# Kernel optimization log

Measured on AMD Instinct MI355X. Metric: run time of the kernel, lower is better.

## Reference

```python
import jax, jax.numpy as jnp
import numpy as np

EPS = 1e-05  # config.norm_eps
C = 4        # len('qkvm')

def setup_inputs() -> dict:
    key = jax.random.key(0)
    k1, k2, k3 = jax.random.split(key, 3)
    B, T, D = 4, 4096, 4096
    L_TOT = 48  # (lidx+2)*C with lidx=10
    x = jax.random.normal(k1, (B, T, D), dtype=jnp.float32)
    # torch Linear weights are [out_features, in_features]
    W1 = jax.random.normal(k2, (L_TOT, D), dtype=jnp.float32) * (D ** -0.5)
    W2 = jax.random.normal(k3, (L_TOT, L_TOT), dtype=jnp.float32) * (L_TOT ** -0.5)
    return {"x": x, "W1": W1, "W2": W2}

def reference(x, W1, W2):
    # RMSNorm without scale
    var = jnp.mean(x * x, axis=-1, keepdims=True)
    xn = x * jax.lax.rsqrt(var + EPS)                      # [B, T, D]
    h = jnp.einsum('btd,ld->btl', xn, W1)                  # [B, T, l]
    dw = jnp.einsum('btk,lk->btl', jax.nn.gelu(h, approximate=False), W2)
    B, T, Ltot = dw.shape
    # rearrange 'B T (C L) -> C B T L'
    return jnp.transpose(dw.reshape(B, T, C, Ltot // C), (2, 0, 1, 3))
```

## Files before the change

kernel.cpp:

```cpp
#include <hip/hip_runtime.h>
#include <hip/hip_bf16.h>

#define DDIM 4096
#define LTOT 48

typedef __attribute__((ext_vector_type(4))) float f32x4;
typedef __attribute__((ext_vector_type(8))) short bf16x8;

__device__ __forceinline__ void gload_lds16(const void* g, void* l) {
    __builtin_amdgcn_global_load_lds(
        (const __attribute__((address_space(1))) void*)g,
        (__attribute__((address_space(3))) void*)l, 16, 0, 0);
}

__device__ __forceinline__ unsigned cvt_pk(float x, float y) {
    union { __hip_bfloat162 h; unsigned u; } c;
    c.h = __float22bfloat162_rn(make_float2(x, y));
    return c.u;
}

__global__ void w1cvt_kernel(const float* __restrict__ w1, ushort* __restrict__ w1b) {
    int i = blockIdx.x * 256 + threadIdx.x;
    union { float f; unsigned u; } v; v.f = w1[i];
    unsigned r = v.u + 0x7fffu + ((v.u >> 16) & 1u);
    w1b[i] = (ushort)(r >> 16);
}

__global__ __launch_bounds__(256, 2) void fused_kernel(
        const float* __restrict__ x,
        const ushort* __restrict__ w1b,
        const float* __restrict__ w2,
        float* __restrict__ out) {
    __shared__ __align__(1024) char smem[65536];
    __shared__ float ssw[4][32];
    __shared__ float scl[32];

    const int tid  = threadIdx.x;
    const int wave = tid >> 6;
    const int lane = tid & 63;
    const int rl   = lane & 15;
    const int kg   = lane >> 4;
    const int row0 = blockIdx.x * 32;
    const int kw   = wave * 1024;
    const int rot  = blockIdx.x & 15;

    char* wbase = smem + wave * 16384;

    int dso[2][2][2];
    #pragma unroll
    for (int T = 0; T < 2; ++T)
        #pragma unroll
        for (int h = 0; h < 2; ++h)
            #pragma unroll
            for (int p = 0; p < 2; ++p)
                dso[T][h][p] = (T * 16 + rl) * 256 + (((h * 8 + kg * 2 + p) ^ rl) << 4);

    auto stage = [&](int t) {
        const int kb = kw + ((t + rot) & 15) * 64;
        char* lb = wbase + (t & 1) * 8192;
        #pragma unroll
        for (int i = 0; i < 8; ++i) {
            int r    = i * 4 + kg;
            int blkg = rl ^ (r & 15);
            const float* src = x + (size_t)(row0 + r) * DDIM + kb + blkg * 4;
            gload_lds16(src, lb + i * 1024);
        }
    };

    auto loadB = [&](int s, bf16x8 (&bl)[6]) {
        const ushort* bp = w1b + (size_t)rl * DDIM + kw + ((s + rot) & 15) * 64 + kg * 8;
        #pragma unroll
        for (int n = 0; n < 3; ++n)
            #pragma unroll
            for (int h = 0; h < 2; ++h)
                bl[n * 2 + h] = *(const bf16x8*)(bp + n * 16 * DDIM + h * 32);
    };

    float ss0 = 0.f, ss1 = 0.f;
    f32x4 acc0[3] = {{0.f,0.f,0.f,0.f},{0.f,0.f,0.f,0.f},{0.f,0.f,0.f,0.f}};
    f32x4 acc1[3] = {{0.f,0.f,0.f,0.f},{0.f,0.f,0.f,0.f},{0.f,0.f,0.f,0.f}};
    bf16x8 bA[6], bB[6];

    stage(0); loadB(0, bA); stage(1);

    auto body = [&](int s, bf16x8 (&bu)[6], bf16x8 (&bl)[6]) {
        if (s == 0)       asm volatile("s_waitcnt vmcnt(14)" ::: "memory");
        else if (s == 15) asm volatile("s_waitcnt vmcnt(6)"  ::: "memory");
        else              asm volatile("s_waitcnt vmcnt(8)"  ::: "memory");
        char* lb = wbase + (s & 1) * 8192;
        f32x4 a[2][2][2];
        #pragma unroll
        for (int T = 0; T < 2; ++T)
            #pragma unroll
            for (int h = 0; h < 2; ++h)
                #pragma unroll
                for (int p = 0; p < 2; ++p)
                    a[T][h][p] = *(const f32x4*)(lb + dso[T][h][p]);
        if (s < 15) loadB(s + 1, bl);
        #pragma unroll
        for (int h = 0; h < 2; ++h) {
            f32x4 a0 = a[0][h][0], a1 = a[0][h][1];
            f32x4 c0 = a[1][h][0], c1 = a[1][h][1];
            ss0 = fmaf(a0.x, a0.x, ss0); ss0 = fmaf(a0.y, a0.y, ss0);
            ss0 = fmaf(a0.z, a0.z, ss0); ss0 = fmaf(a0.w, a0.w, ss0);
            ss0 = fmaf(a1.x, a1.x, ss0); ss0 = fmaf(a1.y, a1.y, ss0);
            ss0 = fmaf(a1.z, a1.z, ss0); ss0 = fmaf(a1.w, a1.w, ss0);
            ss1 = fmaf(c0.x, c0.x, ss1); ss1 = fmaf(c0.y, c0.y, ss1);
            ss1 = fmaf(c0.z, c0.z, ss1); ss1 = fmaf(c0.w, c0.w, ss1);
            ss1 = fmaf(c1.x, c1.x, ss1); ss1 = fmaf(c1.y, c1.y, ss1);
            ss1 = fmaf(c1.z, c1.z, ss1); ss1 = fmaf(c1.w, c1.w, ss1);
            union { bf16x8 v; unsigned u[4]; } af, ag;
            af.u[0] = cvt_pk(a0.x, a0.y); af.u[1] = cvt_pk(a0.z, a0.w);
            af.u[2] = cvt_pk(a1.x, a1.y); af.u[3] = cvt_pk(a1.z, a1.w);
            ag.u[0] = cvt_pk(c0.x, c0.y); ag.u[1] = cvt_pk(c0.z, c0.w);
            ag.u[2] = cvt_pk(c1.x, c1.y); ag.u[3] = cvt_pk(c1.z, c1.w);
            #pragma unroll
            for (int n = 0; n < 3; ++n) {
                acc0[n] = __builtin_amdgcn_mfma_f32_16x16x32_bf16(
                              af.v, bu[n * 2 + h], acc0[n], 0, 0, 0);
                acc1[n] = __builtin_amdgcn_mfma_f32_16x16x32_bf16(
                              ag.v, bu[n * 2 + h], acc1[n], 0, 0, 0);
            }
        }
        asm volatile("s_waitcnt lgkmcnt(0)" ::: "memory");
        if (s < 14) stage(s + 2);
    };

    for (int sp = 0; sp < 8; ++sp) {
        body(2 * sp,     bA, bB);
        body(2 * sp + 1, bB, bA);
    }

    ss0 += __shfl_xor(ss0, 16); ss0 += __shfl_xor(ss0, 32);
    ss1 += __shfl_xor(ss1, 16); ss1 += __shfl_xor(ss1, 32);
    if (lane < 16) { ssw[wave][lane] = ss0; ssw[wave][16 + lane] = ss1; }

    asm volatile("s_waitcnt vmcnt(0) lgkmcnt(0)" ::: "memory");
    __syncthreads();

    float* dots = (float*)smem;
    float* gbuf = (float*)(smem + 24576);
    float* w2s  = (float*)(smem + 30720);

    #pragma unroll
    for (int n = 0; n < 3; ++n)
        #pragma unroll
        for (int i = 0; i < 4; ++i) {
            dots[(wave * 32 + kg * 4 + i) * 48 + n * 16 + rl]      = acc0[n][i];
            dots[(wave * 32 + 16 + kg * 4 + i) * 48 + n * 16 + rl] = acc1[n][i];
        }
    for (int i = tid; i < LTOT * LTOT; i += 256) w2s[i] = w2[i];
    if (tid < 32) {
        float st = ssw[0][tid] + ssw[1][tid] + ssw[2][tid] + ssw[3][tid];
        scl[tid] = rsqrtf(st * (1.0f / (float)DDIM) + 1e-5f);
    }
    __syncthreads();

    #pragma unroll
    for (int i = 0; i < 6; ++i) {
        int v = tid + i * 256;
        int row = v / 48, col = v - row * 48;
        float d = dots[(0 * 32 + row) * 48 + col] + dots[(1 * 32 + row) * 48 + col]
                + dots[(2 * 32 + row) * 48 + col] + dots[(3 * 32 + row) * 48 + col];
        float h = d * scl[row];
        gbuf[row * 48 + col] = h * 0.5f * (1.0f + erff(h * 0.70710678118654752f));
    }
    __syncthreads();

    #pragma unroll
    for (int i = 0; i < 6; ++i) {
        int v = tid + i * 256;
        int row = v / 48, l = v - row * 48;
        float sacc = 0.f;
        #pragma unroll
        for (int k = 0; k < LTOT; ++k)
            sacc = fmaf(gbuf[row * 48 + k], w2s[l * LTOT + k], sacc);
        int rg = row0 + row;
        int b  = rg >> 12;
        int t  = rg & 4095;
        int c  = l / 12, j = l - c * 12;
        out[(((size_t)(c * 4 + b) * 4096 + t) * 12) + j] = sacc;
    }
}

extern "C" void kernel_launch(void* const* d_in, const int* in_sizes, int n_in,
                              void* d_out, int out_size, void* d_ws, size_t ws_size,
                              hipStream_t stream) {
    const float* x  = (const float*)d_in[0];
    const float* W1 = (const float*)d_in[1];
    const float* W2 = (const float*)d_in[2];
    float* out = (float*)d_out;
    ushort* w1b = (ushort*)d_ws;

    w1cvt_kernel<<<(LTOT * DDIM) / 256, 256, 0, stream>>>(W1, w1b);
    fused_kernel<<<16384 / 32, 256, 0, stream>>>(x, w1b, W2, out);
}
```

Before: 58.07 us.

## Stage x tiles through registers into a single-buffered LDS bridge

Replaces the direct global-to-LDS async loads and the double-buffered 64 KB LDS staging with register prefetch: two chunks of x are held in registers and written into a smaller per-wave LDS buffer after each compute step. W1 fragments are now loaded directly in each iteration instead of being prefetched one step ahead, and the hand-written waitcnt instructions are dropped in favour of compiler scheduling. The smaller LDS footprint is meant to allow more resident blocks per CU. The cost is more VGPR pressure from the register staging buffers, extra LDS write instructions, and W1 load latency that is no longer hidden by a prefetch.

```diff
diff --git a/kernel.cpp b/kernel.cpp
--- a/kernel.cpp
+++ b/kernel.cpp
@@ -6,12 +6,6 @@
 
 typedef __attribute__((ext_vector_type(4))) float f32x4;
 typedef __attribute__((ext_vector_type(8))) short bf16x8;
-
-__device__ __forceinline__ void gload_lds16(const void* g, void* l) {
-    __builtin_amdgcn_global_load_lds(
-        (const __attribute__((address_space(1))) void*)g,
-        (__attribute__((address_space(3))) void*)l, 16, 0, 0);
-}
 
 __device__ __forceinline__ unsigned cvt_pk(float x, float y) {
     union { __hip_bfloat162 h; unsigned u; } c;
@@ -31,9 +25,7 @@
         const ushort* __restrict__ w1b,
         const float* __restrict__ w2,
         float* __restrict__ out) {
-    __shared__ __align__(1024) char smem[65536];
-    __shared__ float ssw[4][32];
-    __shared__ float scl[32];
+    __shared__ __align__(1024) char smem[40576];
 
     const int tid  = threadIdx.x;
     const int wave = tid >> 6;
@@ -44,63 +36,71 @@
     const int kw   = wave * 1024;
     const int rot  = blockIdx.x & 15;
 
-    char* wbase = smem + wave * 16384;
+    char*  bridge = smem + wave * 8192;
+    float* ssw    = (float*)(smem + 39936);
+    float* scl    = ssw + 128;
 
-    int dso[2][2][2];
+    int dwo[8];
+    #pragma unroll
+    for (int j = 0; j < 8; ++j) {
+        int r = 4 * j + kg;
+        dwo[j] = r * 256 + (((rl ^ r) & 15) << 4);
+    }
+    int dro[2][2][2];
     #pragma unroll
     for (int T = 0; T < 2; ++T)
         #pragma unroll
-        for (int h = 0; h < 2; ++h)
+        for (int t = 0; t < 2; ++t)
             #pragma unroll
-            for (int p = 0; p < 2; ++p)
-                dso[T][h][p] = (T * 16 + rl) * 256 + (((h * 8 + kg * 2 + p) ^ rl) << 4);
+            for (int p = 0; p < 2; ++p) {
+                int r = T * 16 + rl;
+                int b = t * 8 + kg * 2 + p;
+                dro[T][t][p] = r * 256 + (((b ^ rl) & 15) << 4);
+            }
 
-    auto stage = [&](int t) {
-        const int kb = kw + ((t + rot) & 15) * 64;
-        char* lb = wbase + (t & 1) * 8192;
+    auto kcol = [&](int c) { return kw + ((c + rot) & 15) * 64; };
+
+    auto loadS = [&](int c, f32x4 (&S)[8]) {
+        const float* base = x + (size_t)row0 * DDIM + kcol(c) + rl * 4;
         #pragma unroll
-        for (int i = 0; i < 8; ++i) {
-            int r    = i * 4 + kg;
-            int blkg = rl ^ (r & 15);
-            const float* src = x + (size_t)(row0 + r) * DDIM + kb + blkg * 4;
-            gload_lds16(src, lb + i * 1024);
-        }
+        for (int j = 0; j < 8; ++j)
+            S[j] = *(const f32x4*)(base + (size_t)(4 * j + kg) * DDIM);
     };
-
-    auto loadB = [&](int s, bf16x8 (&bl)[6]) {
-        const ushort* bp = w1b + (size_t)rl * DDIM + kw + ((s + rot) & 15) * 64 + kg * 8;
+    auto writeS = [&](f32x4 (&S)[8]) {
         #pragma unroll
-        for (int n = 0; n < 3; ++n)
-            #pragma unroll
-            for (int h = 0; h < 2; ++h)
-                bl[n * 2 + h] = *(const bf16x8*)(bp + n * 16 * DDIM + h * 32);
+        for (int j = 0; j < 8; ++j)
+            *(f32x4*)(bridge + dwo[j]) = S[j];
     };
 
     float ss0 = 0.f, ss1 = 0.f;
     f32x4 acc0[3] = {{0.f,0.f,0.f,0.f},{0.f,0.f,0.f,0.f},{0.f,0.f,0.f,0.f}};
     f32x4 acc1[3] = {{0.f,0.f,0.f,0.f},{0.f,0.f,0.f,0.f},{0.f,0.f,0.f,0.f}};
-    bf16x8 bA[6], bB[6];
+    f32x4 SA[8], SB[8];
 
-    stage(0); loadB(0, bA); stage(1);
+    loadS(0, SA); loadS(1, SB);
+    writeS(SA);
 
-    auto body = [&](int s, bf16x8 (&bu)[6], bf16x8 (&bl)[6]) {
-        if (s == 0)       asm volatile("s_waitcnt vmcnt(14)" ::: "memory");
-        else if (s == 15) asm volatile("s_waitcnt vmcnt(6)"  ::: "memory");
-        else              asm volatile("s_waitcnt vmcnt(8)"  ::: "memory");
-        char* lb = wbase + (s & 1) * 8192;
+    auto body = [&](int c, f32x4 (&Sld)[8], f32x4 (&Swr)[8]) {
         f32x4 a[2][2][2];
         #pragma unroll
         for (int T = 0; T < 2; ++T)
             #pragma unroll
-            for (int h = 0; h < 2; ++h)
+            for (int t = 0; t < 2; ++t)
                 #pragma unroll
                 for (int p = 0; p < 2; ++p)
-                    a[T][h][p] = *(const f32x4*)(lb + dso[T][h][p]);
-        if (s < 15) loadB(s + 1, bl);
+                    a[T][t][p] = *(const f32x4*)(bridge + dro[T][t][p]);
+        bf16x8 Bf[2][3];
         #pragma unroll
-        for (int h = 0; h < 2; ++h) {
-            f32x4 a0 = a[0][h][0], a1 = a[0][h][1];
-            f32x4 c0 = a[1][h][0], c1 = a[1][h][1];
+        for (int t = 0; t < 2; ++t)
+            #pragma unroll
+            for (int n = 0; n < 3; ++n)
+                Bf[t][n] = *(const bf16x8*)(w1b + (size_t)(n * 16 + rl) * DDIM
+                                            + kcol(c) + t * 32 + kg * 8);
+        if (c < 14) loadS(c + 2, Sld);
+        #pragma unroll
+        for (int t = 0; t < 2; ++t) {
+            f32x4 a0 = a[0][t][0], a1 = a[0][t][1];
+            f32x4 c0 = a[1][t][0], c1 = a[1][t][1];
             ss0 = fmaf(a0.x, a0.x, ss0); ss0 = fmaf(a0.y, a0.y, ss0);
             ss0 = fmaf(a0.z, a0.z, ss0); ss0 = fmaf(a0.w, a0.w, ss0);
             ss0 = fmaf(a1.x, a1.x, ss0); ss0 = fmaf(a1.y, a1.y, ss0);
@@ -117,25 +117,22 @@
             #pragma unroll
             for (int n = 0; n < 3; ++n) {
                 acc0[n] = __builtin_amdgcn_mfma_f32_16x16x32_bf16(
-                              af.v, bu[n * 2 + h], acc0[n], 0, 0, 0);
+                              af.v, Bf[t][n], acc0[n], 0, 0, 0);
                 acc1[n] = __builtin_amdgcn_mfma_f32_16x16x32_bf16(
-                              ag.v, bu[n * 2 + h], acc1[n], 0, 0, 0);
+                              ag.v, Bf[t][n], acc1[n], 0, 0, 0);
             }
         }
-        asm volatile("s_waitcnt lgkmcnt(0)" ::: "memory");
-        if (s < 14) stage(s + 2);
+        if (c < 15) writeS(Swr);
     };
 
     for (int sp = 0; sp < 8; ++sp) {
-        body(2 * sp,     bA, bB);
-        body(2 * sp + 1, bB, bA);
+        body(2 * sp,     SA, SB);
+        body(2 * sp + 1, SB, SA);
     }
 
     ss0 += __shfl_xor(ss0, 16); ss0 += __shfl_xor(ss0, 32);
     ss1 += __shfl_xor(ss1, 16); ss1 += __shfl_xor(ss1, 32);
-    if (lane < 16) { ssw[wave][lane] = ss0; ssw[wave][16 + lane] = ss1; }
-
-    asm volatile("s_waitcnt vmcnt(0) lgkmcnt(0)" ::: "memory");
+    if (lane < 16) { ssw[wave * 32 + lane] = ss0; ssw[wave * 32 + 16 + lane] = ss1; }
     __syncthreads();
 
     float* dots = (float*)smem;
@@ -151,7 +148,7 @@
         }
     for (int i = tid; i < LTOT * LTOT; i += 256) w2s[i] = w2[i];
     if (tid < 32) {
-        float st = ssw[0][tid] + ssw[1][tid] + ssw[2][tid] + ssw[3][tid];
+        float st = ssw[tid] + ssw[32 + tid] + ssw[64 + tid] + ssw[96 + tid];
         scl[tid] = rsqrtf(st * (1.0f / (float)DDIM) + 1e-5f);
     }
     __syncthreads();
@@ -160,8 +157,8 @@
     for (int i = 0; i < 6; ++i) {
         int v = tid + i * 256;
         int row = v / 48, col = v - row * 48;
-        float d = dots[(0 * 32 + row) * 48 + col] + dots[(1 * 32 + row) * 48 + col]
-                + dots[(2 * 32 + row) * 48 + col] + dots[(3 * 32 + row) * 48 + col];
+        float d = dots[row * 48 + col]        + dots[(32 + row) * 48 + col]
+                + dots[(64 + row) * 48 + col] + dots[(96 + row) * 48 + col];
         float h = d * scl[row];
         gbuf[row * 48 + col] = h * 0.5f * (1.0f + erff(h * 0.70710678118654752f));
     }
```

After: 67.48 us. 1.16x slower.
